# Kernel optimization log

Hardware: AMD Instinct MI355X
Metric: run time of the kernel (lower is better)

The kernel has to match this reference:

```python
import jax, jax.numpy as jnp
import numpy as np

WS = (8, 8)          # window_size
HEADS = 8
DH = 64              # dim_head
SHIFT = (4, 4)
SCALE = DH ** -0.5


def setup_inputs() -> dict:
    key = jax.random.key(0)
    ks = jax.random.split(key, 5)
    dim = 64
    inner = HEADS * DH  # 512
    b, h, w = 4, 192, 192
    x = jax.random.normal(ks[0], (b, h, w, dim), dtype=jnp.float32)
    Wq = jax.random.normal(ks[1], (dim, inner), dtype=jnp.float32) * (dim ** -0.5)
    Wkv = jax.random.normal(ks[2], (dim, 2 * inner), dtype=jnp.float32) * (dim ** -0.5)
    Wo = jax.random.normal(ks[3], (inner, dim), dtype=jnp.float32) * (inner ** -0.5)
    bo = jnp.zeros((dim,), dtype=jnp.float32)
    seq_l = WS[0] * WS[1]
    pos_emb = jax.random.normal(ks[4], (1, HEADS, seq_l, seq_l), dtype=jnp.float32)
    return {"x": x, "Wq": Wq, "Wkv": Wkv, "Wo": Wo, "bo": bo, "pos_emb": pos_emb}


def reference(x, Wq, Wkv, Wo, bo, pos_emb):
    b, h, w, c = x.shape
    L = WS[0] * WS[1]  # 64 tokens per window
    if SHIFT[0] > 0:
        x = jnp.roll(x, shift=(-SHIFT[0], -SHIFT[1]), axis=(1, 2))
    # NOTE: original uses a raw .view() here (row-major reshape), NOT an 8x8
    # window partition. Replicate exactly.
    nw = b * (h // WS[0]) * (w // WS[1])
    x_inp = x.reshape(nw, L, c)                      # [nw, 64, c]
    q = x_inp @ Wq                                   # [nw, 64, inner]
    kv = x_inp @ Wkv
    k, v = jnp.split(kv, 2, axis=-1)
    # original: raw view (nw, L, inner) -> (nw, heads, L, dh) (not a transpose)
    q = q.reshape(nw, HEADS, L, DH) * SCALE
    k = k.reshape(nw, HEADS, L, DH)
    v = v.reshape(nw, HEADS, L, DH)
    sim = jnp.einsum('bhid,bhjd->bhij', q, k) + pos_emb
    attn = jax.nn.softmax(sim, axis=-1)
    out = jnp.einsum('bhij,bhjd->bhid', attn, v)     # [nw, heads, 64, dh]
    # original: raw view back to (nw, L, inner)
    out = out.reshape(nw, L, HEADS * DH)
    out = out @ Wo + bo                              # [nw, 64, c]
    out = out.reshape(b, h, w, c)
    if SHIFT[0] > 0:
        out = jnp.roll(out, shift=(SHIFT[0], SHIFT[1]), axis=(1, 2))
    return out
```

## Files before the change

kernel.cpp:

```cpp
#include <hip/hip_runtime.h>
#include <stdint.h>

typedef __attribute__((ext_vector_type(8))) short bf16x8;
typedef __attribute__((ext_vector_type(4))) short s16x4;
typedef __attribute__((ext_vector_type(4))) float f32x4;

#define THREADS 256
constexpr int NWIN = 2304;

constexpr int WCATT_E = 0;
constexpr int WOT_E   = 98304;
constexpr int POS_E   = 131072;
constexpr size_t WS_NEED = 327680;

__device__ __forceinline__ short f2bf(float f) {
  uint32_t u = __builtin_bit_cast(uint32_t, f);
  u += 0x7fffu + ((u >> 16) & 1u);
  return (short)(u >> 16);
}
__device__ __forceinline__ float bf2f(short s) {
  uint32_t u = ((uint32_t)(uint16_t)s) << 16;
  return __builtin_bit_cast(float, u);
}
__device__ __forceinline__ int swz(int row, int h) {
  return ((((row ^ (row >> 2) ^ (row >> 3)) & 7) ^ h) << 4);
}

__global__ void wmsa_prep(const float* __restrict__ Wq, const float* __restrict__ Wkv,
                          const float* __restrict__ Wo, const float* __restrict__ pos,
                          short* __restrict__ ws) {
  int idx = blockIdx.x * 256 + threadIdx.x;
  if (idx < 32768) {
    int n = idx & 511, k = idx >> 9;
    ws[WCATT_E + n * 64 + k] = f2bf(Wq[k * 512 + n] * 0.125f);
  } else if (idx < 98304) {
    int j = idx - 32768;
    int nkv = j & 1023, k = j >> 10;
    ws[WCATT_E + (512 + nkv) * 64 + k] = f2bf(Wkv[k * 1024 + nkv]);
  } else if (idx < 131072) {
    int j = idx - 98304;
    int n = j & 63, k = j >> 6;
    ws[WOT_E + n * 512 + k] = f2bf(Wo[k * 64 + n]);
  } else if (idx < 163840) {
    int j = idx - 131072;
    ws[POS_E + j] = f2bf(pos[j]);
  }
}

__global__ __launch_bounds__(512, 2)
void wmsa_mfma4(const float* __restrict__ x, const float* __restrict__ bo,
                const short* __restrict__ ws, float* __restrict__ out) {
  extern __shared__ __align__(16) char lds[];
  const int tid = threadIdx.x;
  const int wv = tid >> 6;
  const int l  = tid & 63;
  const int lr = l & 15;
  const int lg = l >> 4;

  const int bid = blockIdx.x;
  const int q   = bid >> 2;
  const int hp  = bid & 3;

  bf16x8 xa[4][2];
  #pragma unroll
  for (int win = 0; win < 4; ++win) {
    int w   = 4 * q + win;
    int bb  = w / 576;
    int rem = (w * 64) % 36864;
    int hh  = rem / 192;
    int ww0 = rem % 192;
    int src_h = (hh + 4) % 192;
    const float* xp = x + (size_t)(bb * 192 + src_h) * 12288;
    int tok = 16 * hp + lr;
    int sw = ww0 + tok + 4; if (sw >= 192) sw -= 192;
    const float* xq = xp + sw * 64;
    #pragma unroll
    for (int ks = 0; ks < 2; ++ks) {
      float4 a = *(const float4*)(xq + ks * 32 + lg * 8);
      float4 b = *(const float4*)(xq + ks * 32 + lg * 8 + 4);
      bf16x8 v;
      v[0] = f2bf(a.x); v[1] = f2bf(a.y); v[2] = f2bf(a.z); v[3] = f2bf(a.w);
      v[4] = f2bf(b.x); v[5] = f2bf(b.y); v[6] = f2bf(b.z); v[7] = f2bf(b.w);
      xa[win][ks] = v;
    }
  }

  #pragma unroll
  for (int t = 0; t < 8; ++t) {
    int nt = wv + 8 * t;
    int nload = nt * 16 + lr;
    bf16x8 b0 = *(const bf16x8*)(ws + WCATT_E + nload * 64 + lg * 8);
    bf16x8 b1 = *(const bf16x8*)(ws + WCATT_E + nload * 64 + 32 + lg * 8);
    const bool isQ = (t < 4);
    int i  = (lr & 7) * 8 + ((nt >> 2) & 7);
    int h2 = lr >> 3;
    int d0 = (nt & 3) * 16 + lg * 4;
    int off = (isQ ? 0 : 16384) + h2 * 8192 + i * 128 + ((d0 * 2) ^ swz(i, h2));
    #pragma unroll
    for (int win = 0; win < 4; ++win) {
      f32x4 acc = {0.f, 0.f, 0.f, 0.f};
      acc = __builtin_amdgcn_mfma_f32_16x16x32_bf16(b0, xa[win][0], acc, 0, 0, 0);
      acc = __builtin_amdgcn_mfma_f32_16x16x32_bf16(b1, xa[win][1], acc, 0, 0, 0);
      s16x4 pk;
      #pragma unroll
      for (int r = 0; r < 4; ++r) pk[r] = f2bf(acc[r]);
      *(s16x4*)(lds + win * 32768 + off) = pk;
    }
  }

  const int bq = wv & 3, aq = wv >> 2;
  f32x4 vacc[4][4];
  #pragma unroll
  for (int u = 0; u < 4; ++u) {
    int ntile = (aq * 4 + u) * 4 + bq;
    int nload = (64 + ntile) * 16 + lr;
    bf16x8 b0 = *(const bf16x8*)(ws + WCATT_E + nload * 64 + lg * 8);
    bf16x8 b1 = *(const bf16x8*)(ws + WCATT_E + nload * 64 + 32 + lg * 8);
    #pragma unroll
    for (int win = 0; win < 4; ++win) {
      f32x4 acc = {0.f, 0.f, 0.f, 0.f};
      acc = __builtin_amdgcn_mfma_f32_16x16x32_bf16(xa[win][0], b0, acc, 0, 0, 0);
      acc = __builtin_amdgcn_mfma_f32_16x16x32_bf16(xa[win][1], b1, acc, 0, 0, 0);
      vacc[win][u] = acc;
    }
  }
  __syncthreads();

  const int hl = (wv >> 1) & 1;
  const int ih = wv & 1;
  const int hglob = 2 * hp + hl;
  const int wbase = aq;

  s16x4 posr[2][4];
  #pragma unroll
  for (int it = 0; it < 2; ++it) {
    int i = (ih * 2 + it) * 16 + lr;
    const short* pp = ws + POS_E + hglob * 4096 + i * 64;
    #pragma unroll
    for (int jt = 0; jt < 4; ++jt)
      posr[it][jt] = *(const s16x4*)(pp + jt * 16 + lg * 4);
  }

  #pragma unroll
  for (int c = 0; c < 2; ++c) {
    char* ldw = lds + (wbase + 2 * c) * 32768;
    f32x4 s[2][4];
    #pragma unroll
    for (int it = 0; it < 2; ++it)
      #pragma unroll
      for (int jt = 0; jt < 4; ++jt) s[it][jt] = (f32x4){0.f, 0.f, 0.f, 0.f};

    #pragma unroll
    for (int ks = 0; ks < 2; ++ks) {
      bf16x8 kb[4], qa[2];
      #pragma unroll
      for (int jt = 0; jt < 4; ++jt) {
        int j = jt * 16 + lr;
        kb[jt] = *(const bf16x8*)(ldw + 16384 + hl * 8192 + j * 128 + ((ks * 64 + lg * 16) ^ swz(j, hl)));
      }
      #pragma unroll
      for (int it = 0; it < 2; ++it) {
        int i = (ih * 2 + it) * 16 + lr;
        qa[it] = *(const bf16x8*)(ldw + hl * 8192 + i * 128 + ((ks * 64 + lg * 16) ^ swz(i, hl)));
      }
      __builtin_amdgcn_s_setprio(1);
      #pragma unroll
      for (int it = 0; it < 2; ++it)
        #pragma unroll
        for (int jt = 0; jt < 4; ++jt)
          s[it][jt] = __builtin_amdgcn_mfma_f32_16x16x32_bf16(kb[jt], qa[it], s[it][jt], 0, 0, 0);
      __builtin_amdgcn_s_setprio(0);
    }

    #pragma unroll
    for (int it = 0; it < 2; ++it) {
      int i = (ih * 2 + it) * 16 + lr;
      float sum = 0.f;
      #pragma unroll
      for (int jt = 0; jt < 4; ++jt)
        #pragma unroll
        for (int r = 0; r < 4; ++r) {
          float pv = __expf(s[it][jt][r] + bf2f(posr[it][jt][r]));
          s[it][jt][r] = pv;
          sum += pv;
        }
      sum += __shfl_xor(sum, 16);
      sum += __shfl_xor(sum, 32);
      float rinv = 1.f / sum;
      #pragma unroll
      for (int jt = 0; jt < 4; ++jt) {
        s16x4 pk;
        #pragma unroll
        for (int r = 0; r < 4; ++r) pk[r] = f2bf(s[it][jt][r] * rinv);
        *(s16x4*)(ldw + hl * 8192 + i * 128 + ((jt * 32 + lg * 8) ^ swz(i, hl))) = pk;
      }
    }
  }
  __syncthreads();

  {
    int d = bq * 16 + lr;
    #pragma unroll
    for (int win = 0; win < 4; ++win)
      #pragma unroll
      for (int r = 0; r < 4; ++r) {
        int tl = lg * 4 + r;
        int h2 = tl >> 3;
        int jb = (tl & 7) * 16 + aq * 8;
        s16x4 pk;
        #pragma unroll
        for (int u = 0; u < 4; ++u) pk[u] = f2bf(vacc[win][u][r]);
        *(s16x4*)(lds + win * 32768 + 16384 + h2 * 8192 + d * 128 + (jb ^ swz(d, h2))) = pk;
      }
  }
  __syncthreads();

  bf16x8 wofr[16];
  #pragma unroll
  for (int ks = 0; ks < 16; ++ks)
    wofr[ks] = *(const bf16x8*)(ws + WOT_E + (bq * 16 + lr) * 512 + ks * 32 + lg * 8);

  #pragma unroll
  for (int c = 0; c < 2; ++c) {
    char* ldw = lds + (wbase + 2 * c) * 32768;
    f32x4 o[2][4];
    #pragma unroll
    for (int it = 0; it < 2; ++it)
      #pragma unroll
      for (int dt = 0; dt < 4; ++dt) o[it][dt] = (f32x4){0.f, 0.f, 0.f, 0.f};
    #pragma unroll
    for (int ks = 0; ks < 2; ++ks) {
      bf16x8 vb[4], pa[2];
      #pragma unroll
      for (int dt = 0; dt < 4; ++dt) {
        int d = dt * 16 + lr;
        vb[dt] = *(const bf16x8*)(ldw + 16384 + hl * 8192 + d * 128 + ((ks * 64 + lg * 16) ^ swz(d, hl)));
      }
      #pragma unroll
      for (int it = 0; it < 2; ++it) {
        int i = (ih * 2 + it) * 16 + lr;
        pa[it] = *(const bf16x8*)(ldw + hl * 8192 + i * 128 + ((ks * 64 + lg * 16) ^ swz(i, hl)));
      }
      __builtin_amdgcn_s_setprio(1);
      #pragma unroll
      for (int it = 0; it < 2; ++it)
        #pragma unroll
        for (int dt = 0; dt < 4; ++dt)
          o[it][dt] = __builtin_amdgcn_mfma_f32_16x16x32_bf16(vb[dt], pa[it], o[it][dt], 0, 0, 0);
      __builtin_amdgcn_s_setprio(0);
    }
    #pragma unroll
    for (int it = 0; it < 2; ++it) {
      int i  = (ih * 2 + it) * 16 + lr;
      int lm = 8 * hl + (i >> 3);
      int rp = lm * 8 + (i & 7);
      #pragma unroll
      for (int dt = 0; dt < 4; ++dt) {
        s16x4 pk;
        #pragma unroll
        for (int r = 0; r < 4; ++r) pk[r] = f2bf(o[it][dt][r]);
        *(s16x4*)(ldw + rp * 128 + ((dt * 32 + lg * 8) ^ swz(rp, 0))) = pk;
      }
    }
  }
  __syncthreads();

  f32x4 oacc0 = {0.f, 0.f, 0.f, 0.f};
  f32x4 oacc1 = {0.f, 0.f, 0.f, 0.f};
  #pragma unroll
  for (int ks = 0; ks < 16; ++ks) {
    int rp = lr * 8 + (ks >> 1);
    int boff = rp * 128 + (((ks & 1) * 64 + lg * 16) ^ swz(rp, 0));
    bf16x8 bA = *(const bf16x8*)(lds + wbase * 32768 + boff);
    bf16x8 bB = *(const bf16x8*)(lds + (wbase + 2) * 32768 + boff);
    oacc0 = __builtin_amdgcn_mfma_f32_16x16x32_bf16(wofr[ks], bA, oacc0, 0, 0, 0);
    oacc1 = __builtin_amdgcn_mfma_f32_16x16x32_bf16(wofr[ks], bB, oacc1, 0, 0, 0);
  }
  {
    int c0 = bq * 16 + lg * 4;
    float4 bo4 = *(const float4*)(bo + c0);
    int tok = 16 * hp + lr;
    #pragma unroll
    for (int c = 0; c < 2; ++c) {
      int w   = 4 * q + wbase + 2 * c;
      int bb  = w / 576;
      int rem = (w * 64) % 36864;
      int hh  = rem / 192;
      int ww0 = rem % 192;
      int src_h = (hh + 4) % 192;
      float* orow = out + (size_t)(bb * 192 + src_h) * 12288;
      int sw = ww0 + tok + 4; if (sw >= 192) sw -= 192;
      f32x4 oa = c ? oacc1 : oacc0;
      float4 ov;
      ov.x = oa[0] + bo4.x; ov.y = oa[1] + bo4.y;
      ov.z = oa[2] + bo4.z; ov.w = oa[3] + bo4.w;
      *(float4*)(orow + sw * 64 + c0) = ov;
    }
  }
}

__global__ __launch_bounds__(THREADS, 2)
void wmsa_mfma(const float* __restrict__ x, const float* __restrict__ bo,
               const short* __restrict__ ws, float* __restrict__ out) {
  __shared__ __align__(16) char lds[65536];
  const int tid = threadIdx.x;
  const int wv = tid >> 6;
  const int l  = tid & 63;
  const int lr = l & 15;
  const int lg = l >> 4;

  const int bid = blockIdx.x;
  const int p   = bid >> 2;
  const int hp  = bid & 3;

  const float* xrow[2];
  float* orow[2];
  int ww0a[2];
  #pragma unroll
  for (int win = 0; win < 2; ++win) {
    int w   = 2 * p + win;
    int t0  = w * 64;
    int bb  = t0 / 36864;
    int rem = t0 % 36864;
    int hh  = rem / 192;
    ww0a[win] = rem % 192;
    int src_h = (hh + 4) % 192;
    xrow[win] = x + (size_t)(bb * 192 + src_h) * 12288;
    orow[win] = out + (size_t)(bb * 192 + src_h) * 12288;
  }

  bf16x8 xa[2][2];
  #pragma unroll
  for (int win = 0; win < 2; ++win) {
    int tok = 16 * hp + lr;
    int sw = ww0a[win] + tok + 4; if (sw >= 192) sw -= 192;
    const float* xp = xrow[win] + sw * 64;
    #pragma unroll
    for (int ks = 0; ks < 2; ++ks) {
      float4 a = *(const float4*)(xp + ks * 32 + lg * 8);
      float4 b = *(const float4*)(xp + ks * 32 + lg * 8 + 4);
      bf16x8 v;
      v[0] = f2bf(a.x); v[1] = f2bf(a.y); v[2] = f2bf(a.z); v[3] = f2bf(a.w);
      v[4] = f2bf(b.x); v[5] = f2bf(b.y); v[6] = f2bf(b.z); v[7] = f2bf(b.w);
      xa[win][ks] = v;
    }
  }

  #pragma unroll 4
  for (int t = 0; t < 16; ++t) {
    int nt = wv + 4 * t;
    int nload = nt * 16 + lr;
    bf16x8 b0 = *(const bf16x8*)(ws + WCATT_E + nload * 64 + lg * 8);
    bf16x8 b1 = *(const bf16x8*)(ws + WCATT_E + nload * 64 + 32 + lg * 8);
    const bool isQ = (t < 8);
    int i  = (lr & 7) * 8 + (t & 7);
    int h2 = lr >> 3;
    int d0 = wv * 16 + lg * 4;
    int off = (isQ ? 0 : 16384) + h2 * 8192 + i * 128 + ((d0 * 2) ^ swz(i, h2));
    #pragma unroll
    for (int win = 0; win < 2; ++win) {
      f32x4 acc = {0.f, 0.f, 0.f, 0.f};
      acc = __builtin_amdgcn_mfma_f32_16x16x32_bf16(b0, xa[win][0], acc, 0, 0, 0);
      acc = __builtin_amdgcn_mfma_f32_16x16x32_bf16(b1, xa[win][1], acc, 0, 0, 0);
      s16x4 pk;
      #pragma unroll
      for (int r = 0; r < 4; ++r) pk[r] = f2bf(acc[r]);
      *(s16x4*)(lds + win * 32768 + off) = pk;
    }
  }

  f32x4 vacc[2][8];
  #pragma unroll
  for (int tv = 0; tv < 8; ++tv) {
    int nload = (64 + wv + 4 * tv) * 16 + lr;
    bf16x8 b0 = *(const bf16x8*)(ws + WCATT_E + nload * 64 + lg * 8);
    bf16x8 b1 = *(const bf16x8*)(ws + WCATT_E + nload * 64 + 32 + lg * 8);
    #pragma unroll
    for (int win = 0; win < 2; ++win) {
      f32x4 acc = {0.f, 0.f, 0.f, 0.f};
      acc = __builtin_amdgcn_mfma_f32_16x16x32_bf16(xa[win][0], b0, acc, 0, 0, 0);
      acc = __builtin_amdgcn_mfma_f32_16x16x32_bf16(xa[win][1], b1, acc, 0, 0, 0);
      vacc[win][tv] = acc;
    }
  }
  __syncthreads();

  const int hl = wv >> 1;
  const int ih = wv & 1;
  const int hglob = 2 * hp + hl;

  s16x4 posr[2][4];
  #pragma unroll
  for (int it = 0; it < 2; ++it) {
    int i = (ih * 2 + it) * 16 + lr;
    const short* pp = ws + POS_E + hglob * 4096 + i * 64;
    #pragma unroll
    for (int jt = 0; jt < 4; ++jt)
      posr[it][jt] = *(const s16x4*)(pp + jt * 16 + lg * 4);
  }

  #pragma unroll
  for (int win = 0; win < 2; ++win) {
    char* ldw = lds + win * 32768;
    f32x4 s[2][4];
    #pragma unroll
    for (int it = 0; it < 2; ++it)
      #pragma unroll
      for (int jt = 0; jt < 4; ++jt) s[it][jt] = (f32x4){0.f, 0.f, 0.f, 0.f};

    #pragma unroll
    for (int ks = 0; ks < 2; ++ks) {
      bf16x8 kb[4], qa[2];
      #pragma unroll
      for (int jt = 0; jt < 4; ++jt) {
        int j = jt * 16 + lr;
        kb[jt] = *(const bf16x8*)(ldw + 16384 + hl * 8192 + j * 128 + ((ks * 64 + lg * 16) ^ swz(j, hl)));
      }
      #pragma unroll
      for (int it = 0; it < 2; ++it) {
        int i = (ih * 2 + it) * 16 + lr;
        qa[it] = *(const bf16x8*)(ldw + hl * 8192 + i * 128 + ((ks * 64 + lg * 16) ^ swz(i, hl)));
      }
      __builtin_amdgcn_s_setprio(1);
      #pragma unroll
      for (int it = 0; it < 2; ++it)
        #pragma unroll
        for (int jt = 0; jt < 4; ++jt)
          s[it][jt] = __builtin_amdgcn_mfma_f32_16x16x32_bf16(kb[jt], qa[it], s[it][jt], 0, 0, 0);
      __builtin_amdgcn_s_setprio(0);
    }

    #pragma unroll
    for (int it = 0; it < 2; ++it) {
      int i = (ih * 2 + it) * 16 + lr;
      float sum = 0.f;
      #pragma unroll
      for (int jt = 0; jt < 4; ++jt)
        #pragma unroll
        for (int r = 0; r < 4; ++r) {
          float pv = __expf(s[it][jt][r] + bf2f(posr[it][jt][r]));
          s[it][jt][r] = pv;
          sum += pv;
        }
      sum += __shfl_xor(sum, 16);
      sum += __shfl_xor(sum, 32);
      float rinv = 1.f / sum;
      #pragma unroll
      for (int jt = 0; jt < 4; ++jt) {
        s16x4 pk;
        #pragma unroll
        for (int r = 0; r < 4; ++r) pk[r] = f2bf(s[it][jt][r] * rinv);
        *(s16x4*)(ldw + hl * 8192 + i * 128 + ((jt * 32 + lg * 8) ^ swz(i, hl))) = pk;
      }
    }
  }
  __syncthreads();

  {
    int d = wv * 16 + lr;
    #pragma unroll
    for (int win = 0; win < 2; ++win)
      #pragma unroll
      for (int r = 0; r < 4; ++r) {
        int tl = lg * 4 + r;
        int h2 = tl >> 3;
        int slot = tl & 7;
        bf16x8 pk;
        #pragma unroll
        for (int tv = 0; tv < 8; ++tv) pk[tv] = f2bf(vacc[win][tv][r]);
        *(bf16x8*)(lds + win * 32768 + 16384 + h2 * 8192 + d * 128 + ((slot * 16) ^ swz(d, h2))) = pk;
      }
  }
  __syncthreads();

  bf16x8 wofr[16];
  #pragma unroll
  for (int ks = 0; ks < 16; ++ks)
    wofr[ks] = *(const bf16x8*)(ws + WOT_E + (wv * 16 + lr) * 512 + ks * 32 + lg * 8);

  #pragma unroll
  for (int win = 0; win < 2; ++win) {
    char* ldw = lds + win * 32768;
    f32x4 o[2][4];
    #pragma unroll
    for (int it = 0; it < 2; ++it)
      #pragma unroll
      for (int dt = 0; dt < 4; ++dt) o[it][dt] = (f32x4){0.f, 0.f, 0.f, 0.f};
    #pragma unroll
    for (int ks = 0; ks < 2; ++ks) {
      bf16x8 vb[4], pa[2];
      #pragma unroll
      for (int dt = 0; dt < 4; ++dt) {
        int d = dt * 16 + lr;
        vb[dt] = *(const bf16x8*)(ldw + 16384 + hl * 8192 + d * 128 + ((ks * 64 + lg * 16) ^ swz(d, hl)));
      }
      #pragma unroll
      for (int it = 0; it < 2; ++it) {
        int i = (ih * 2 + it) * 16 + lr;
        pa[it] = *(const bf16x8*)(ldw + hl * 8192 + i * 128 + ((ks * 64 + lg * 16) ^ swz(i, hl)));
      }
      __builtin_amdgcn_s_setprio(1);
      #pragma unroll
      for (int it = 0; it < 2; ++it)
        #pragma unroll
        for (int dt = 0; dt < 4; ++dt)
          o[it][dt] = __builtin_amdgcn_mfma_f32_16x16x32_bf16(vb[dt], pa[it], o[it][dt], 0, 0, 0);
      __builtin_amdgcn_s_setprio(0);
    }
    #pragma unroll
    for (int it = 0; it < 2; ++it) {
      int i  = (ih * 2 + it) * 16 + lr;
      int lm = 8 * hl + (i >> 3);
      int rp = lm * 8 + (i & 7);
      #pragma unroll
      for (int dt = 0; dt < 4; ++dt) {
        s16x4 pk;
        #pragma unroll
        for (int r = 0; r < 4; ++r) pk[r] = f2bf(o[it][dt][r]);
        *(s16x4*)(ldw + rp * 128 + ((dt * 32 + lg * 8) ^ swz(rp, 0))) = pk;
      }
    }
  }
  __syncthreads();

  f32x4 oacc[2];
  oacc[0] = (f32x4){0.f, 0.f, 0.f, 0.f};
  oacc[1] = (f32x4){0.f, 0.f, 0.f, 0.f};
  #pragma unroll
  for (int ks = 0; ks < 16; ++ks) {
    int rp = lr * 8 + (ks >> 1);
    int boff = rp * 128 + (((ks & 1) * 64 + lg * 16) ^ swz(rp, 0));
    #pragma unroll
    for (int win = 0; win < 2; ++win) {
      bf16x8 bfrOH = *(const bf16x8*)(lds + win * 32768 + boff);
      oacc[win] = __builtin_amdgcn_mfma_f32_16x16x32_bf16(wofr[ks], bfrOH, oacc[win], 0, 0, 0);
    }
  }
  {
    int c0 = wv * 16 + lg * 4;
    float4 bo4 = *(const float4*)(bo + c0);
    int tok = 16 * hp + lr;
    #pragma unroll
    for (int win = 0; win < 2; ++win) {
      int sw = ww0a[win] + tok + 4; if (sw >= 192) sw -= 192;
      float4 ov;
      ov.x = oacc[win][0] + bo4.x; ov.y = oacc[win][1] + bo4.y;
      ov.z = oacc[win][2] + bo4.z; ov.w = oacc[win][3] + bo4.w;
      *(float4*)(orow[win] + sw * 64 + c0) = ov;
    }
  }
}

extern "C" void kernel_launch(void* const* d_in, const int* in_sizes, int n_in,
                              void* d_out, int out_size, void* d_ws, size_t ws_size,
                              hipStream_t stream) {
  const float* x    = (const float*)d_in[0];
  const float* Wq   = (const float*)d_in[1];
  const float* Wkv  = (const float*)d_in[2];
  const float* Wo   = (const float*)d_in[3];
  const float* bo   = (const float*)d_in[4];
  const float* pos  = (const float*)d_in[5];
  float* o = (float*)d_out;
  if (ws_size >= WS_NEED) {
    wmsa_prep<<<dim3(640), dim3(256), 0, stream>>>(Wq, Wkv, Wo, pos, (short*)d_ws);
    hipError_t e = hipFuncSetAttribute((const void*)wmsa_mfma4,
                                       hipFuncAttributeMaxDynamicSharedMemorySize, 131072);
    if (e == hipSuccess) {
      wmsa_mfma4<<<dim3(NWIN), dim3(512), 131072, stream>>>(x, bo, (const short*)d_ws, o);
    } else {
      wmsa_mfma<<<dim3(NWIN * 2), dim3(THREADS), 0, stream>>>(x, bo, (const short*)d_ws, o);
    }
  } else {
    wmsa_prep<<<dim3(640), dim3(256), 0, stream>>>(Wq, Wkv, Wo, pos, (short*)d_ws);
    wmsa_mfma<<<dim3(NWIN * 2), dim3(THREADS), 0, stream>>>(x, bo, (const short*)d_ws, o);
  }
}
```

Measured before the change: 179.8 us.

## Make windowed attention kernel persistent with register-prefetched next quad of x

```diff
diff --git a/kernel.cpp b/kernel.cpp
--- a/kernel.cpp
+++ b/kernel.cpp
@@ -47,26 +47,13 @@
   }
 }
 
-__global__ __launch_bounds__(512, 2)
-void wmsa_mfma4(const float* __restrict__ x, const float* __restrict__ bo,
-                const short* __restrict__ ws, float* __restrict__ out) {
-  extern __shared__ __align__(16) char lds[];
-  const int tid = threadIdx.x;
-  const int wv = tid >> 6;
-  const int l  = tid & 63;
-  const int lr = l & 15;
-  const int lg = l >> 4;
-
-  const int bid = blockIdx.x;
-  const int q   = bid >> 2;
-  const int hp  = bid & 3;
-
-  bf16x8 xa[4][2];
+__device__ __forceinline__ void load_xa(const float* __restrict__ x, int quad, int hp,
+                                        int lr, int lg, bf16x8 (&xa)[4][2]) {
   #pragma unroll
   for (int win = 0; win < 4; ++win) {
-    int w   = 4 * q + win;
+    int w   = quad * 4 + win;
     int bb  = w / 576;
-    int rem = (w * 64) % 36864;
+    int rem = (w % 576) * 64;
     int hh  = rem / 192;
     int ww0 = rem % 192;
     int src_h = (hh + 4) % 192;
@@ -84,48 +71,22 @@
       xa[win][ks] = v;
     }
   }
-
-  #pragma unroll
-  for (int t = 0; t < 8; ++t) {
-    int nt = wv + 8 * t;
-    int nload = nt * 16 + lr;
-    bf16x8 b0 = *(const bf16x8*)(ws + WCATT_E + nload * 64 + lg * 8);
-    bf16x8 b1 = *(const bf16x8*)(ws + WCATT_E + nload * 64 + 32 + lg * 8);
-    const bool isQ = (t < 4);
-    int i  = (lr & 7) * 8 + ((nt >> 2) & 7);
-    int h2 = lr >> 3;
-    int d0 = (nt & 3) * 16 + lg * 4;
-    int off = (isQ ? 0 : 16384) + h2 * 8192 + i * 128 + ((d0 * 2) ^ swz(i, h2));
-    #pragma unroll
-    for (int win = 0; win < 4; ++win) {
-      f32x4 acc = {0.f, 0.f, 0.f, 0.f};
-      acc = __builtin_amdgcn_mfma_f32_16x16x32_bf16(b0, xa[win][0], acc, 0, 0, 0);
-      acc = __builtin_amdgcn_mfma_f32_16x16x32_bf16(b1, xa[win][1], acc, 0, 0, 0);
-      s16x4 pk;
-      #pragma unroll
-      for (int r = 0; r < 4; ++r) pk[r] = f2bf(acc[r]);
-      *(s16x4*)(lds + win * 32768 + off) = pk;
-    }
-  }
+}
+
+__global__ __launch_bounds__(512, 2)
+void wmsa_pers(const float* __restrict__ x, const float* __restrict__ bo,
+               const short* __restrict__ ws, float* __restrict__ out) {
+  extern __shared__ __align__(16) char lds[];
+  const int tid = threadIdx.x;
+  const int wv = tid >> 6;
+  const int l  = tid & 63;
+  const int lr = l & 15;
+  const int lg = l >> 4;
+
+  const int qg = blockIdx.x >> 2;
+  const int hp = blockIdx.x & 3;
 
   const int bq = wv & 3, aq = wv >> 2;
-  f32x4 vacc[4][4];
-  #pragma unroll
-  for (int u = 0; u < 4; ++u) {
-    int ntile = (aq * 4 + u) * 4 + bq;
-    int nload = (64 + ntile) * 16 + lr;
-    bf16x8 b0 = *(const bf16x8*)(ws + WCATT_E + nload * 64 + lg * 8);
-    bf16x8 b1 = *(const bf16x8*)(ws + WCATT_E + nload * 64 + 32 + lg * 8);
-    #pragma unroll
-    for (int win = 0; win < 4; ++win) {
-      f32x4 acc = {0.f, 0.f, 0.f, 0.f};
-      acc = __builtin_amdgcn_mfma_f32_16x16x32_bf16(xa[win][0], b0, acc, 0, 0, 0);
-      acc = __builtin_amdgcn_mfma_f32_16x16x32_bf16(xa[win][1], b1, acc, 0, 0, 0);
-      vacc[win][u] = acc;
-    }
-  }
-  __syncthreads();
-
   const int hl = (wv >> 1) & 1;
   const int ih = wv & 1;
   const int hglob = 2 * hp + hl;
@@ -133,168 +94,224 @@
 
   s16x4 posr[2][4];
   #pragma unroll
-  for (int it = 0; it < 2; ++it) {
-    int i = (ih * 2 + it) * 16 + lr;
+  for (int it2 = 0; it2 < 2; ++it2) {
+    int i = (ih * 2 + it2) * 16 + lr;
     const short* pp = ws + POS_E + hglob * 4096 + i * 64;
     #pragma unroll
     for (int jt = 0; jt < 4; ++jt)
-      posr[it][jt] = *(const s16x4*)(pp + jt * 16 + lg * 4);
-  }
-
-  #pragma unroll
-  for (int c = 0; c < 2; ++c) {
-    char* ldw = lds + (wbase + 2 * c) * 32768;
-    f32x4 s[2][4];
-    #pragma unroll
-    for (int it = 0; it < 2; ++it)
-      #pragma unroll
-      for (int jt = 0; jt < 4; ++jt) s[it][jt] = (f32x4){0.f, 0.f, 0.f, 0.f};
-
-    #pragma unroll
-    for (int ks = 0; ks < 2; ++ks) {
-      bf16x8 kb[4], qa[2];
-      #pragma unroll
-      for (int jt = 0; jt < 4; ++jt) {
-        int j = jt * 16 + lr;
-        kb[jt] = *(const bf16x8*)(ldw + 16384 + hl * 8192 + j * 128 + ((ks * 64 + lg * 16) ^ swz(j, hl)));
-      }
-      #pragma unroll
-      for (int it = 0; it < 2; ++it) {
-        int i = (ih * 2 + it) * 16 + lr;
-        qa[it] = *(const bf16x8*)(ldw + hl * 8192 + i * 128 + ((ks * 64 + lg * 16) ^ swz(i, hl)));
-      }
-      __builtin_amdgcn_s_setprio(1);
-      #pragma unroll
-      for (int it = 0; it < 2; ++it)
+      posr[it2][jt] = *(const s16x4*)(pp + jt * 16 + lg * 4);
+  }
+
+  bf16x8 xaA[4][2], xaB[4][2];
+  load_xa(x, qg * 9, hp, lr, lg, xaA);
+
+  for (int it = 0; it < 9; ++it) {
+    const int quad = qg * 9 + it;
+
+    #pragma unroll
+    for (int t = 0; t < 8; ++t) {
+      int nt = wv + 8 * t;
+      int nload = nt * 16 + lr;
+      bf16x8 b0 = *(const bf16x8*)(ws + WCATT_E + nload * 64 + lg * 8);
+      bf16x8 b1 = *(const bf16x8*)(ws + WCATT_E + nload * 64 + 32 + lg * 8);
+      const bool isQ = (t < 4);
+      int i  = (lr & 7) * 8 + ((nt >> 2) & 7);
+      int h2 = lr >> 3;
+      int d0 = (nt & 3) * 16 + lg * 4;
+      int off = (isQ ? 0 : 16384) + h2 * 8192 + i * 128 + ((d0 * 2) ^ swz(i, h2));
+      #pragma unroll
+      for (int win = 0; win < 4; ++win) {
+        f32x4 acc = {0.f, 0.f, 0.f, 0.f};
+        acc = __builtin_amdgcn_mfma_f32_16x16x32_bf16(b0, xaA[win][0], acc, 0, 0, 0);
+        acc = __builtin_amdgcn_mfma_f32_16x16x32_bf16(b1, xaA[win][1], acc, 0, 0, 0);
+        s16x4 pk;
+        #pragma unroll
+        for (int r = 0; r < 4; ++r) pk[r] = f2bf(acc[r]);
+        *(s16x4*)(lds + win * 32768 + off) = pk;
+      }
+    }
+
+    f32x4 vacc[4][4];
+    #pragma unroll
+    for (int u = 0; u < 4; ++u) {
+      int ntile = (aq * 4 + u) * 4 + bq;
+      int nload = (64 + ntile) * 16 + lr;
+      bf16x8 b0 = *(const bf16x8*)(ws + WCATT_E + nload * 64 + lg * 8);
+      bf16x8 b1 = *(const bf16x8*)(ws + WCATT_E + nload * 64 + 32 + lg * 8);
+      #pragma unroll
+      for (int win = 0; win < 4; ++win) {
+        f32x4 acc = {0.f, 0.f, 0.f, 0.f};
+        acc = __builtin_amdgcn_mfma_f32_16x16x32_bf16(xaA[win][0], b0, acc, 0, 0, 0);
+        acc = __builtin_amdgcn_mfma_f32_16x16x32_bf16(xaA[win][1], b1, acc, 0, 0, 0);
+        vacc[win][u] = acc;
+      }
+    }
+    __syncthreads();
+
+    #pragma unroll
+    for (int c = 0; c < 2; ++c) {
+      char* ldw = lds + (wbase + 2 * c) * 32768;
+      f32x4 s[2][4];
+      #pragma unroll
+      for (int it2 = 0; it2 < 2; ++it2)
+        #pragma unroll
+        for (int jt = 0; jt < 4; ++jt) s[it2][jt] = (f32x4){0.f, 0.f, 0.f, 0.f};
+
+      #pragma unroll
+      for (int ks = 0; ks < 2; ++ks) {
+        bf16x8 kb[4], qa[2];
+        #pragma unroll
+        for (int jt = 0; jt < 4; ++jt) {
+          int j = jt * 16 + lr;
+          kb[jt] = *(const bf16x8*)(ldw + 16384 + hl * 8192 + j * 128 + ((ks * 64 + lg * 16) ^ swz(j, hl)));
+        }
+        #pragma unroll
+        for (int it2 = 0; it2 < 2; ++it2) {
+          int i = (ih * 2 + it2) * 16 + lr;
+          qa[it2] = *(const bf16x8*)(ldw + hl * 8192 + i * 128 + ((ks * 64 + lg * 16) ^ swz(i, hl)));
+        }
+        __builtin_amdgcn_s_setprio(1);
+        #pragma unroll
+        for (int it2 = 0; it2 < 2; ++it2)
+          #pragma unroll
+          for (int jt = 0; jt < 4; ++jt)
+            s[it2][jt] = __builtin_amdgcn_mfma_f32_16x16x32_bf16(kb[jt], qa[it2], s[it2][jt], 0, 0, 0);
+        __builtin_amdgcn_s_setprio(0);
+      }
+
+      #pragma unroll
+      for (int it2 = 0; it2 < 2; ++it2) {
+        int i = (ih * 2 + it2) * 16 + lr;
+        float sum = 0.f;
         #pragma unroll
         for (int jt = 0; jt < 4; ++jt)
-          s[it][jt] = __builtin_amdgcn_mfma_f32_16x16x32_bf16(kb[jt], qa[it], s[it][jt], 0, 0, 0);
-      __builtin_amdgcn_s_setprio(0);
-    }
-
-    #pragma unroll
-    for (int it = 0; it < 2; ++it) {
-      int i = (ih * 2 + it) * 16 + lr;
-      float sum = 0.f;
-      #pragma unroll
-      for (int jt = 0; jt < 4; ++jt)
+          #pragma unroll
+          for (int r = 0; r < 4; ++r) {
+            float pv = __expf(s[it2][jt][r] + bf2f(posr[it2][jt][r]));
+            s[it2][jt][r] = pv;
+            sum += pv;
+          }
+        sum += __shfl_xor(sum, 16);
+        sum += __shfl_xor(sum, 32);
+        float rinv = 1.f / sum;
+        #pragma unroll
+        for (int jt = 0; jt < 4; ++jt) {
+          s16x4 pk;
+          #pragma unroll
+          for (int r = 0; r < 4; ++r) pk[r] = f2bf(s[it2][jt][r] * rinv);
+          *(s16x4*)(ldw + hl * 8192 + i * 128 + ((jt * 32 + lg * 8) ^ swz(i, hl))) = pk;
+        }
+      }
+    }
+    __syncthreads();
+
+    {
+      int d = bq * 16 + lr;
+      #pragma unroll
+      for (int win = 0; win < 4; ++win)
         #pragma unroll
         for (int r = 0; r < 4; ++r) {
-          float pv = __expf(s[it][jt][r] + bf2f(posr[it][jt][r]));
-          s[it][jt][r] = pv;
-          sum += pv;
-        }
-      sum += __shfl_xor(sum, 16);
-      sum += __shfl_xor(sum, 32);
-      float rinv = 1.f / sum;
-      #pragma unroll
-      for (int jt = 0; jt < 4; ++jt) {
-        s16x4 pk;
-        #pragma unroll
-        for (int r = 0; r < 4; ++r) pk[r] = f2bf(s[it][jt][r] * rinv);
-        *(s16x4*)(ldw + hl * 8192 + i * 128 + ((jt * 32 + lg * 8) ^ swz(i, hl))) = pk;
-      }
-    }
-  }
-  __syncthreads();
-
-  {
-    int d = bq * 16 + lr;
-    #pragma unroll
-    for (int win = 0; win < 4; ++win)
-      #pragma unroll
-      for (int r = 0; r < 4; ++r) {
-        int tl = lg * 4 + r;
-        int h2 = tl >> 3;
-        int jb = (tl & 7) * 16 + aq * 8;
-        s16x4 pk;
-        #pragma unroll
-        for (int u = 0; u < 4; ++u) pk[u] = f2bf(vacc[win][u][r]);
-        *(s16x4*)(lds + win * 32768 + 16384 + h2 * 8192 + d * 128 + (jb ^ swz(d, h2))) = pk;
-      }
-  }
-  __syncthreads();
-
-  bf16x8 wofr[16];
-  #pragma unroll
-  for (int ks = 0; ks < 16; ++ks)
-    wofr[ks] = *(const bf16x8*)(ws + WOT_E + (bq * 16 + lr) * 512 + ks * 32 + lg * 8);
-
-  #pragma unroll
-  for (int c = 0; c < 2; ++c) {
-    char* ldw = lds + (wbase + 2 * c) * 32768;
-    f32x4 o[2][4];
-    #pragma unroll
-    for (int it = 0; it < 2; ++it)
-      #pragma unroll
-      for (int dt = 0; dt < 4; ++dt) o[it][dt] = (f32x4){0.f, 0.f, 0.f, 0.f};
-    #pragma unroll
-    for (int ks = 0; ks < 2; ++ks) {
-      bf16x8 vb[4], pa[2];
-      #pragma unroll
-      for (int dt = 0; dt < 4; ++dt) {
-        int d = dt * 16 + lr;
-        vb[dt] = *(const bf16x8*)(ldw + 16384 + hl * 8192 + d * 128 + ((ks * 64 + lg * 16) ^ swz(d, hl)));
-      }
-      #pragma unroll
-      for (int it = 0; it < 2; ++it) {
-        int i = (ih * 2 + it) * 16 + lr;
-        pa[it] = *(const bf16x8*)(ldw + hl * 8192 + i * 128 + ((ks * 64 + lg * 16) ^ swz(i, hl)));
-      }
-      __builtin_amdgcn_s_setprio(1);
-      #pragma unroll
-      for (int it = 0; it < 2; ++it)
-        #pragma unroll
-        for (int dt = 0; dt < 4; ++dt)
-          o[it][dt] = __builtin_amdgcn_mfma_f32_16x16x32_bf16(vb[dt], pa[it], o[it][dt], 0, 0, 0);
-      __builtin_amdgcn_s_setprio(0);
-    }
-    #pragma unroll
-    for (int it = 0; it < 2; ++it) {
-      int i  = (ih * 2 + it) * 16 + lr;
-      int lm = 8 * hl + (i >> 3);
-      int rp = lm * 8 + (i & 7);
-      #pragma unroll
-      for (int dt = 0; dt < 4; ++dt) {
-        s16x4 pk;
-        #pragma unroll
-        for (int r = 0; r < 4; ++r) pk[r] = f2bf(o[it][dt][r]);
-        *(s16x4*)(ldw + rp * 128 + ((dt * 32 + lg * 8) ^ swz(rp, 0))) = pk;
-      }
-    }
-  }
-  __syncthreads();
-
-  f32x4 oacc0 = {0.f, 0.f, 0.f, 0.f};
-  f32x4 oacc1 = {0.f, 0.f, 0.f, 0.f};
-  #pragma unroll
-  for (int ks = 0; ks < 16; ++ks) {
-    int rp = lr * 8 + (ks >> 1);
-    int boff = rp * 128 + (((ks & 1) * 64 + lg * 16) ^ swz(rp, 0));
-    bf16x8 bA = *(const bf16x8*)(lds + wbase * 32768 + boff);
-    bf16x8 bB = *(const bf16x8*)(lds + (wbase + 2) * 32768 + boff);
-    oacc0 = __builtin_amdgcn_mfma_f32_16x16x32_bf16(wofr[ks], bA, oacc0, 0, 0, 0);
-    oacc1 = __builtin_amdgcn_mfma_f32_16x16x32_bf16(wofr[ks], bB, oacc1, 0, 0, 0);
-  }
-  {
-    int c0 = bq * 16 + lg * 4;
-    float4 bo4 = *(const float4*)(bo + c0);
-    int tok = 16 * hp + lr;
+          int tl = lg * 4 + r;
+          int h2 = tl >> 3;
+          int jb = (tl & 7) * 16 + aq * 8;
+          s16x4 pk;
+          #pragma unroll
+          for (int u = 0; u < 4; ++u) pk[u] = f2bf(vacc[win][u][r]);
+          *(s16x4*)(lds + win * 32768 + 16384 + h2 * 8192 + d * 128 + (jb ^ swz(d, h2))) = pk;
+        }
+    }
+    __syncthreads();
+
+    bf16x8 wofr[16];
+    #pragma unroll
+    for (int ks = 0; ks < 16; ++ks)
+      wofr[ks] = *(const bf16x8*)(ws + WOT_E + (bq * 16 + lr) * 512 + ks * 32 + lg * 8);
+
+    if (it < 8) load_xa(x, quad + 1, hp, lr, lg, xaB);
+
     #pragma unroll
     for (int c = 0; c < 2; ++c) {
-      int w   = 4 * q + wbase + 2 * c;
-      int bb  = w / 576;
-      int rem = (w * 64) % 36864;
-      int hh  = rem / 192;
-      int ww0 = rem % 192;
-      int src_h = (hh + 4) % 192;
-      float* orow = out + (size_t)(bb * 192 + src_h) * 12288;
-      int sw = ww0 + tok + 4; if (sw >= 192) sw -= 192;
-      f32x4 oa = c ? oacc1 : oacc0;
-      float4 ov;
-      ov.x = oa[0] + bo4.x; ov.y = oa[1] + bo4.y;
-      ov.z = oa[2] + bo4.z; ov.w = oa[3] + bo4.w;
-      *(float4*)(orow + sw * 64 + c0) = ov;
+      char* ldw = lds + (wbase + 2 * c) * 32768;
+      f32x4 o[2][4];
+      #pragma unroll
+      for (int it2 = 0; it2 < 2; ++it2)
+        #pragma unroll
+        for (int dt = 0; dt < 4; ++dt) o[it2][dt] = (f32x4){0.f, 0.f, 0.f, 0.f};
+      #pragma unroll
+      for (int ks = 0; ks < 2; ++ks) {
+        bf16x8 vb[4], pa[2];
+        #pragma unroll
+        for (int dt = 0; dt < 4; ++dt) {
+          int d = dt * 16 + lr;
+          vb[dt] = *(const bf16x8*)(ldw + 16384 + hl * 8192 + d * 128 + ((ks * 64 + lg * 16) ^ swz(d, hl)));
+        }
+        #pragma unroll
+        for (int it2 = 0; it2 < 2; ++it2) {
+          int i = (ih * 2 + it2) * 16 + lr;
+          pa[it2] = *(const bf16x8*)(ldw + hl * 8192 + i * 128 + ((ks * 64 + lg * 16) ^ swz(i, hl)));
+        }
+        __builtin_amdgcn_s_setprio(1);
+        #pragma unroll
+        for (int it2 = 0; it2 < 2; ++it2)
+          #pragma unroll
+          for (int dt = 0; dt < 4; ++dt)
+            o[it2][dt] = __builtin_amdgcn_mfma_f32_16x16x32_bf16(vb[dt], pa[it2], o[it2][dt], 0, 0, 0);
+        __builtin_amdgcn_s_setprio(0);
+      }
+      #pragma unroll
+      for (int it2 = 0; it2 < 2; ++it2) {
+        int i  = (ih * 2 + it2) * 16 + lr;
+        int lm = 8 * hl + (i >> 3);
+        int rp = lm * 8 + (i & 7);
+        #pragma unroll
+        for (int dt = 0; dt < 4; ++dt) {
+          s16x4 pk;
+          #pragma unroll
+          for (int r = 0; r < 4; ++r) pk[r] = f2bf(o[it2][dt][r]);
+          *(s16x4*)(ldw + rp * 128 + ((dt * 32 + lg * 8) ^ swz(rp, 0))) = pk;
+        }
+      }
+    }
+    __syncthreads();
+
+    f32x4 oacc0 = {0.f, 0.f, 0.f, 0.f};
+    f32x4 oacc1 = {0.f, 0.f, 0.f, 0.f};
+    #pragma unroll
+    for (int ks = 0; ks < 16; ++ks) {
+      int rp = lr * 8 + (ks >> 1);
+      int boff = rp * 128 + (((ks & 1) * 64 + lg * 16) ^ swz(rp, 0));
+      bf16x8 bA = *(const bf16x8*)(lds + wbase * 32768 + boff);
+      bf16x8 bB = *(const bf16x8*)(lds + (wbase + 2) * 32768 + boff);
+      oacc0 = __builtin_amdgcn_mfma_f32_16x16x32_bf16(wofr[ks], bA, oacc0, 0, 0, 0);
+      oacc1 = __builtin_amdgcn_mfma_f32_16x16x32_bf16(wofr[ks], bB, oacc1, 0, 0, 0);
+    }
+    {
+      int c0 = bq * 16 + lg * 4;
+      float4 bo4 = *(const float4*)(bo + c0);
+      int tok = 16 * hp + lr;
+      #pragma unroll
+      for (int c = 0; c < 2; ++c) {
+        int w   = quad * 4 + wbase + 2 * c;
+        int bb  = w / 576;
+        int rem = (w % 576) * 64;
+        int hh  = rem / 192;
+        int ww0 = rem % 192;
+        int src_h = (hh + 4) % 192;
+        float* orow = out + (size_t)(bb * 192 + src_h) * 12288;
+        int sw = ww0 + tok + 4; if (sw >= 192) sw -= 192;
+        f32x4 oa = c ? oacc1 : oacc0;
+        float4 ov;
+        ov.x = oa[0] + bo4.x; ov.y = oa[1] + bo4.y;
+        ov.z = oa[2] + bo4.z; ov.w = oa[3] + bo4.w;
+        *(float4*)(orow + sw * 64 + c0) = ov;
+      }
+    }
+    __syncthreads();
+
+    #pragma unroll
+    for (int win = 0; win < 4; ++win) {
+      xaA[win][0] = xaB[win][0];
+      xaA[win][1] = xaB[win][1];
     }
   }
 }
@@ -561,17 +578,12 @@
   const float* bo   = (const float*)d_in[4];
   const float* pos  = (const float*)d_in[5];
   float* o = (float*)d_out;
-  if (ws_size >= WS_NEED) {
-    wmsa_prep<<<dim3(640), dim3(256), 0, stream>>>(Wq, Wkv, Wo, pos, (short*)d_ws);
-    hipError_t e = hipFuncSetAttribute((const void*)wmsa_mfma4,
-                                       hipFuncAttributeMaxDynamicSharedMemorySize, 131072);
-    if (e == hipSuccess) {
-      wmsa_mfma4<<<dim3(NWIN), dim3(512), 131072, stream>>>(x, bo, (const short*)d_ws, o);
-    } else {
-      wmsa_mfma<<<dim3(NWIN * 2), dim3(THREADS), 0, stream>>>(x, bo, (const short*)d_ws, o);
-    }
+  wmsa_prep<<<dim3(640), dim3(256), 0, stream>>>(Wq, Wkv, Wo, pos, (short*)d_ws);
+  hipError_t e = hipFuncSetAttribute((const void*)wmsa_pers,
+                                     hipFuncAttributeMaxDynamicSharedMemorySize, 131072);
+  if (e == hipSuccess) {
+    wmsa_pers<<<dim3(256), dim3(512), 131072, stream>>>(x, bo, (const short*)d_ws, o);
   } else {
-    wmsa_prep<<<dim3(640), dim3(256), 0, stream>>>(Wq, Wkv, Wo, pos, (short*)d_ws);
     wmsa_mfma<<<dim3(NWIN * 2), dim3(THREADS), 0, stream>>>(x, bo, (const short*)d_ws, o);
   }
 }
```

Result: slower. 299.6 us (+66.6%).
